# Kernel tuning notes

Hardware: AMD Instinct MI355X
Metric: run time of the kernel (lower is better)

Reference implementation:

```python
import jax, jax.numpy as jnp
from jax import lax
import numpy as np

# ITA requantization params (from init_kwargs)
MQ, SQ = 16384, 8
MK, SK = 16384, 8
MV, SV = 16384, 8
MA, SA = 5, 12
MAV, SAV = 1, 8
MO, SO = 256, 7
NUM_HEADS = 6


def requantize(x, mult, shift, add=0):
    # x * mult, floor-div by 2**shift, add, clamp to int8 range (values kept in float32)
    return jnp.clip(jnp.floor(x * mult / (2.0 ** shift)) + add, -128.0, 127.0)


def ita_softmax(x):
    # x: [B, h, S, Skv] float32 with integer values in [-128, 127]
    B, h, S, Skv = x.shape
    width, bits = 16, 8
    eps_max = 32.0 * bits / (2 ** bits)  # range_scale * bits / 2**bits = 1.0
    groups = Skv // width
    x3 = x.reshape(B * h, S, Skv).astype(jnp.int32)
    # [groups, BH, S, width] for streaming scan over key chunks
    chunks = x3.reshape(B * h, S, groups, width).transpose(2, 0, 1, 3)

    def step(carry, chunk):
        exp_partial_sum, global_max = carry
        current_max = chunk.max(axis=-1)
        update = current_max > global_max
        max_shift = jnp.floor((current_max - global_max).astype(jnp.float32) * eps_max + 0.5).astype(jnp.int32)
        shift_sum = jnp.where(update, max_shift, 0)
        global_max = jnp.where(update, current_max, global_max)
        diff = global_max[..., None] - chunk  # >= 0
        shift = jnp.floor(diff.astype(jnp.float32) * eps_max + 0.5).astype(jnp.int32)
        # 2**bits >> shift  (256 >> shift; any shift >= 9 yields 0, clamp to keep shift defined)
        exp_sum = jnp.sum(jnp.right_shift(jnp.int32(256), jnp.minimum(shift, 31)), axis=-1).astype(jnp.int32)
        exp_partial_sum = jnp.right_shift(exp_partial_sum, jnp.minimum(shift_sum, 31)) + exp_sum
        return (exp_partial_sum, global_max), None

    init = (jnp.zeros((B * h, S), jnp.int32), jnp.full((B * h, S), -128, jnp.int32))
    (exp_partial_sum, global_max), _ = lax.scan(step, init, chunks)

    # (2**bits - 1) * 2**bits = 65280
    inv = jnp.floor(65280.0 / exp_partial_sum.astype(jnp.float32)).astype(jnp.int32)
    diff = global_max[..., None] - x3  # >= 0
    shift = jnp.floor(diff.astype(jnp.float32) * eps_max + 0.5).astype(jnp.int32)
    res = jnp.right_shift(inv[..., None], jnp.minimum(shift, 31)).astype(jnp.uint8)
    return res.reshape(B, h, S, Skv)


def setup_inputs() -> dict:
    key = jax.random.key(0)
    ks = jax.random.split(key, 9)
    B, N, D = 4, 2048, 384
    scale = 1.0 / np.sqrt(D)
    return {
        "x": jax.random.normal(ks[0], (B, N, D), jnp.float32),
        "wq": jax.random.normal(ks[1], (D, D), jnp.float32) * scale,
        "bq": jnp.zeros((D,), jnp.float32),
        "wk": jax.random.normal(ks[2], (D, D), jnp.float32) * scale,
        "bk": jnp.zeros((D,), jnp.float32),
        "wv": jax.random.normal(ks[3], (D, D), jnp.float32) * scale,
        "bv": jnp.zeros((D,), jnp.float32),
        "wo": jax.random.normal(ks[4], (D, D), jnp.float32) * scale,
        "bo": jnp.zeros((D,), jnp.float32),
        "H": 64,
        "W": 32,
    }


def reference(x, wq, bq, wk, bk, wv, bv, wo, bo, H, W):
    B, N, _ = x.shape
    h = NUM_HEADS
    hd = wq.shape[0] // h

    Q = requantize(x @ wq.T + bq, MQ, SQ)
    K = requantize(x @ wk.T + bk, MK, SK)
    V = requantize(x @ wv.T + bv, MV, SV)

    Qr = Q.reshape(B, N, h, hd).transpose(0, 2, 1, 3)  # [B,h,N,hd]
    Kr = K.reshape(B, N, h, hd).transpose(0, 2, 1, 3)
    Vr = V.reshape(B, N, h, hd).transpose(0, 2, 1, 3)

    logits = requantize(jnp.einsum('bhqd,bhkd->bhqk', Qr, Kr), MA, SA)
    attn = ita_softmax(logits)  # uint8 [B,h,N,N]
    ctx = requantize(jnp.einsum('bhqk,bhkd->bhqd', attn.astype(jnp.float32), Vr), MAV, SAV)
    ctx = ctx.transpose(0, 2, 1, 3).reshape(B, N, h * hd)
    out = requantize(ctx @ wo.T + bo, MO, SO)
    return out
```

## Files before the change

### kernel.cpp

```cpp
#include <hip/hip_runtime.h>
#include <stdint.h>

#define NB 4
#define NN 2048
#define ND 384
#define NH 6
#define HD 64
#define ROWS (NB * NN)

typedef int v4i __attribute__((ext_vector_type(4)));
typedef float v4f __attribute__((ext_vector_type(4)));
typedef float v2f __attribute__((ext_vector_type(2)));
typedef _Float16 half_t;
typedef half_t v8h __attribute__((ext_vector_type(8)));

#define PK_FMA_LO(accv, ap, bp)                                            \
    asm("v_pk_fma_f32 %0, %1, %2, %0 op_sel:[0,0,0] op_sel_hi:[0,1,1]"     \
        : "+v"(accv) : "v"(ap), "v"(bp))
#define PK_FMA_HI(accv, ap, bp)                                            \
    asm("v_pk_fma_f32 %0, %1, %2, %0 op_sel:[1,0,0] op_sel_hi:[1,1,1]"     \
        : "+v"(accv) : "v"(ap), "v"(bp))

__global__ __launch_bounds__(256) void qkv_gemm_kernel(
    const float* __restrict__ X,
    const float* __restrict__ Wq, const float* __restrict__ Wk, const float* __restrict__ Wv,
    const float* __restrict__ Bq, const float* __restrict__ Bk, const float* __restrict__ Bv,
    int8_t* __restrict__ Q8, int8_t* __restrict__ K8, int8_t* __restrict__ V8T,
    int* __restrict__ CS)
{
    __shared__ __attribute__((aligned(16))) float As[2][16][132];
    __shared__ __attribute__((aligned(16))) float Bs[2][16][100];
    __shared__ int lcol[96];

    const int t = threadIdx.x;
    const int tx = t & 15;
    const int ty = t >> 4;
    const int row0 = blockIdx.x * 128;
    const int m = blockIdx.y >> 2;
    const int cl0 = (blockIdx.y & 3) * 96;
    const float* W = (m == 0) ? Wq : (m == 1) ? Wk : Wv;
    const float* Bi = (m == 0) ? Bq : (m == 1) ? Bk : Bv;

    const int sr = t >> 1;
    const int sk = (t & 1) * 8;
    const float* xp = X + (size_t)(row0 + sr) * ND + sk;
    const float* wp = W + (size_t)(cl0 + sr) * ND + sk;

    v2f acc[8][3];
#pragma unroll
    for (int i = 0; i < 8; ++i)
#pragma unroll
        for (int p = 0; p < 3; ++p) acc[i][p] = (v2f)0.0f;

    float4 xa0 = *(const float4*)xp;
    float4 xa1 = *(const float4*)(xp + 4);
    float4 wb0, wb1;
    if (t < 192) { wb0 = *(const float4*)wp; wb1 = *(const float4*)(wp + 4); }

    int cur = 0;
    for (int k0 = 0; k0 < ND; k0 += 16) {
        As[cur][sk + 0][sr] = xa0.x; As[cur][sk + 1][sr] = xa0.y;
        As[cur][sk + 2][sr] = xa0.z; As[cur][sk + 3][sr] = xa0.w;
        As[cur][sk + 4][sr] = xa1.x; As[cur][sk + 5][sr] = xa1.y;
        As[cur][sk + 6][sr] = xa1.z; As[cur][sk + 7][sr] = xa1.w;
        if (t < 192) {
            Bs[cur][sk + 0][sr] = wb0.x; Bs[cur][sk + 1][sr] = wb0.y;
            Bs[cur][sk + 2][sr] = wb0.z; Bs[cur][sk + 3][sr] = wb0.w;
            Bs[cur][sk + 4][sr] = wb1.x; Bs[cur][sk + 5][sr] = wb1.y;
            Bs[cur][sk + 6][sr] = wb1.z; Bs[cur][sk + 7][sr] = wb1.w;
        }

        if (k0 + 16 < ND) {
            xa0 = *(const float4*)(xp + k0 + 16);
            xa1 = *(const float4*)(xp + k0 + 20);
            if (t < 192) {
                wb0 = *(const float4*)(wp + k0 + 16);
                wb1 = *(const float4*)(wp + k0 + 20);
            }
        }
        __syncthreads();

#pragma unroll
        for (int kk = 0; kk < 16; ++kk) {
            const v2f* arp  = (const v2f*)&As[cur][kk][ty * 8];
            const v2f* brp  = (const v2f*)&Bs[cur][kk][tx * 4];
            const v2f* brp2 = (const v2f*)&Bs[cur][kk][64 + tx * 2];
            v2f ap0 = arp[0], ap1 = arp[1], ap2 = arp[2], ap3 = arp[3];
            v2f bp0 = brp[0], bp1 = brp[1], bp2 = brp2[0];

            PK_FMA_LO(acc[0][0], ap0, bp0); PK_FMA_LO(acc[0][1], ap0, bp1);
            PK_FMA_LO(acc[0][2], ap0, bp2);
            PK_FMA_HI(acc[1][0], ap0, bp0); PK_FMA_HI(acc[1][1], ap0, bp1);
            PK_FMA_HI(acc[1][2], ap0, bp2);

            PK_FMA_LO(acc[2][0], ap1, bp0); PK_FMA_LO(acc[2][1], ap1, bp1);
            PK_FMA_LO(acc[2][2], ap1, bp2);
            PK_FMA_HI(acc[3][0], ap1, bp0); PK_FMA_HI(acc[3][1], ap1, bp1);
            PK_FMA_HI(acc[3][2], ap1, bp2);

            PK_FMA_LO(acc[4][0], ap2, bp0); PK_FMA_LO(acc[4][1], ap2, bp1);
            PK_FMA_LO(acc[4][2], ap2, bp2);
            PK_FMA_HI(acc[5][0], ap2, bp0); PK_FMA_HI(acc[5][1], ap2, bp1);
            PK_FMA_HI(acc[5][2], ap2, bp2);

            PK_FMA_LO(acc[6][0], ap3, bp0); PK_FMA_LO(acc[6][1], ap3, bp1);
            PK_FMA_LO(acc[6][2], ap3, bp2);
            PK_FMA_HI(acc[7][0], ap3, bp0); PK_FMA_HI(acc[7][1], ap3, bp1);
            PK_FMA_HI(acc[7][2], ap3, bp2);
        }
        cur ^= 1;
    }

    const int bidx = row0 >> 11;
    const int n0 = row0 & 2047;
    const int c1 = cl0 + tx * 4;
    const int c2 = cl0 + 64 + tx * 2;
    const int h1 = c1 >> 6, d1 = c1 & 63;
    const int h2 = c2 >> 6, d2 = c2 & 63;

    if (m != 2) {
        int8_t* Out = (m == 0) ? Q8 : K8;
        const float b1a = Bi[c1], b1b = Bi[c1 + 1], b1c = Bi[c1 + 2], b1d = Bi[c1 + 3];
        const float b2a = Bi[c2], b2b = Bi[c2 + 1];
#pragma unroll
        for (int i = 0; i < 8; ++i) {
            const int n = n0 + ty * 8 + i;
            float v0 = acc[i][0][0] + b1a, v1 = acc[i][0][1] + b1b;
            float v2 = acc[i][1][0] + b1c, v3 = acc[i][1][1] + b1d;
            int q0 = max(-128, min(127, (int)floorf(v0 * 64.0f)));
            int q1 = max(-128, min(127, (int)floorf(v1 * 64.0f)));
            int q2 = max(-128, min(127, (int)floorf(v2 * 64.0f)));
            int q3 = max(-128, min(127, (int)floorf(v3 * 64.0f)));
            uint32_t w = (uint32_t)(q0 & 255) | ((uint32_t)(q1 & 255) << 8)
                       | ((uint32_t)(q2 & 255) << 16) | ((uint32_t)(q3 & 255) << 24);
            *(uint32_t*)(Out + (((size_t)(bidx * NH + h1) * NN) + n) * HD + d1) = w;

            float v4 = acc[i][2][0] + b2a, v5 = acc[i][2][1] + b2b;
            int q4 = max(-128, min(127, (int)floorf(v4 * 64.0f)));
            int q5 = max(-128, min(127, (int)floorf(v5 * 64.0f)));
            *(uint16_t*)(Out + (((size_t)(bidx * NH + h2) * NN) + n) * HD + d2) =
                (uint16_t)((q4 & 255) | ((q5 & 255) << 8));
        }
    } else {
        if (t < 96) lcol[t] = 0;
        __syncthreads();
#pragma unroll
        for (int j = 0; j < 6; ++j) {
            const int lc = (j < 4) ? (tx * 4 + j) : (64 + tx * 2 + (j - 4));
            const int col = cl0 + lc;
            const int head = col >> 6, d = col & 63;
            const float bias = Bi[col];
            int s = 0;
            uint32_t w[2] = {0u, 0u};
#pragma unroll
            for (int i = 0; i < 8; ++i) {
                float v = ((j < 4) ? acc[i][j >> 1][j & 1] : acc[i][2][j - 4]) + bias;
                int qv = (int)floorf(v * 64.0f);
                qv = max(-128, min(127, qv));
                s += qv;
                w[i >> 2] |= (uint32_t)(qv & 255) << (8 * (i & 3));
            }
            uint32_t* dst = (uint32_t*)(V8T + ((size_t)(bidx * NH + head) * HD + d) * NN
                                        + n0 + ty * 8);
            dst[0] = w[0];
            dst[1] = w[1];
            atomicAdd(&lcol[lc], s);
        }
        __syncthreads();
        if (t < 96) {
            const int col = cl0 + t;
            atomicAdd(&CS[(bidx * NH + (col >> 6)) * 64 + (col & 63)], lcol[t]);
        }
    }
}

__global__ __launch_bounds__(256, 4) void attn_kernel(
    const int8_t* __restrict__ Q8, const int8_t* __restrict__ K8,
    const int8_t* __restrict__ V8T, const int* __restrict__ colsum,
    int8_t* __restrict__ CTX8)
{
    __shared__ int Lp[128 * 68];
    __shared__ int gmaxw[128 * 4];
    __shared__ int esumw[128 * 8];

    const int t = threadIdx.x;
    const int wid = t >> 6;
    const int lane = t & 63;
    const int quad = lane >> 4;
    const int l15 = lane & 15;
    const int bh = blockIdx.y;
    const int q0 = blockIdx.x * 16;
    const size_t base = (size_t)bh * NN * HD;
    const v4i zero = {0, 0, 0, 0};

    v4i afrag = *(const v4i*)(Q8 + base + (size_t)(q0 + l15) * HD + quad * 16);
    {
        const int8_t* kp = K8 + base + (size_t)(wid * 32 * 16 + l15) * HD + quad * 16;
        v4i bfrag = *(const v4i*)kp;
        for (int kt = wid * 32; kt < wid * 32 + 32; ++kt) {
            v4i cur = bfrag;
            kp += 16 * HD;
            bfrag = *(const v4i*)kp;
            v4i d = __builtin_amdgcn_mfma_i32_16x16x64_i8(afrag, cur, zero, 0, 0, 0);
            int e[4];
#pragma unroll
            for (int r = 0; r < 4; ++r) {
                int lg = (d[r] * 5) >> 12;
                e[r] = min(127, max(-128, lg));
            }
            int p01 = __builtin_amdgcn_perm(e[1], e[0], 0x00000400);
            int p23 = __builtin_amdgcn_perm(e[3], e[2], 0x00000400);
            Lp[kt * 68 + quad * 16 + l15] = __builtin_amdgcn_perm(p23, p01, 0x05040100);
        }
    }
    __syncthreads();

    int wb[2][16];
#pragma unroll
    for (int it = 0; it < 2; ++it) {
        const int task = t + it * 256;
        const int g = task & 127, qq = task >> 7;
        const int* p = &Lp[g * 68 + qq * 16];
#pragma unroll
        for (int a = 0; a < 4; ++a) {
            v4i v = *(const v4i*)&p[a * 4];
            wb[it][a * 4 + 0] = v.x; wb[it][a * 4 + 1] = v.y;
            wb[it][a * 4 + 2] = v.z; wb[it][a * 4 + 3] = v.w;
        }
        int mx[4];
#pragma unroll
        for (int b = 0; b < 4; ++b) {
            int m = INT_MIN;
#pragma unroll
            for (int j = 0; j < 16; ++j)
                m = max(m, (int)((unsigned)wb[it][j] << (8 * (3 - b))));
            mx[b] = m;
        }
        int p01 = __builtin_amdgcn_perm(mx[1], mx[0], 0x00000703);
        int p23 = __builtin_amdgcn_perm(mx[3], mx[2], 0x00000703);
        gmaxw[g * 4 + qq] = __builtin_amdgcn_perm(p23, p01, 0x05040100);
    }
    __syncthreads();

    if (t < 16) {
        const int wq = t >> 2, bq = 8 * (t & 3);
        int8_t* gb = (int8_t*)gmaxw;
        int m = -128;
        for (int g = 0; g < 128; ++g) {
            int x = (int)(int8_t)(gmaxw[g * 4 + wq] >> bq);
            m = max(m, x);
            gb[g * 16 + t] = (int8_t)m;
        }
    }
    __syncthreads();

#pragma unroll
    for (int it = 0; it < 2; ++it) {
        const int task = t + it * 256;
        const int g = task & 127, qq = task >> 7;
        const int pw = gmaxw[g * 4 + qq];
        uint32_t sp[2] = {0u, 0u};
#pragma unroll
        for (int b = 0; b < 4; ++b) {
            const int M = (int)(int8_t)(pw >> (8 * b));
            const int cb = 8 - M;
            int s = 0;
#pragma unroll
            for (int j = 0; j < 16; ++j) {
                int x = (int)(int8_t)(wb[it][j] >> (8 * b));
                int tt = x + cb;
                s += (tt >= 0) ? (1 << tt) : 0;
            }
            sp[b >> 1] |= (uint32_t)s << (16 * (b & 1));
        }
        *(int2*)&esumw[g * 8 + qq * 2] = make_int2((int)sp[0], (int)sp[1]);
    }
    __syncthreads();

    if (t < 16) {
        const int8_t* gb = (const int8_t*)gmaxw;
        const uint16_t* eb = (const uint16_t*)esumw;
        int E = 0, Mp = -128;
        for (int g = 0; g < 128; ++g) {
            int m = (int)gb[g * 16 + t];
            int d = m - Mp; if (d > 31) d = 31;
            E = (E >> d) + (int)eb[g * 16 + t];
            Mp = m;
        }
        Lp[t * 68 + 64] = 65280 / E;
        Lp[t * 68 + 65] = Mp;
    }
    __syncthreads();

    const int inv_l = Lp[l15 * 68 + 64];
    const int c24 = 24 - Lp[l15 * 68 + 65];
    const int sh8 = 8 * (l15 & 3);
    v4i accs[4] = {zero, zero, zero, zero};
    const int8_t* vtb = V8T + base;

    v4i bf[4];
    {
        const int koff0 = wid * 8 * 64 + quad * 16;
#pragma unroll
        for (int dtb = 0; dtb < 4; ++dtb)
            bf[dtb] = *(const v4i*)(vtb + (size_t)(dtb * 16 + l15) * NN + koff0);
    }
    for (int kc = wid * 8; kc < wid * 8 + 8; ++kc) {
        const int* lp = &Lp[(kc * 4 + quad) * 68 + (l15 >> 2) * 16];
        v4i w4[4];
#pragma unroll
        for (int r = 0; r < 4; ++r) w4[r] = *(const v4i*)&lp[4 * r];

        v4i b0 = bf[0], b1 = bf[1], b2 = bf[2], b3 = bf[3];
        const int koffn = (kc + 1) * 64 + quad * 16;
#pragma unroll
        for (int dtb = 0; dtb < 4; ++dtb)
            bf[dtb] = *(const v4i*)(vtb + (size_t)(dtb * 16 + l15) * NN + koffn);

        v4i a;
#pragma unroll
        for (int r = 0; r < 4; ++r) {
            int u[4];
#pragma unroll
            for (int c = 0; c < 4; ++c) {
                int x = (int)(int8_t)(w4[r][c] >> sh8);
                int t1 = x + c24;
                t1 = (t1 < 0) ? 0 : t1;
                u[c] = (int)((unsigned)inv_l << t1);
            }
            int p01 = __builtin_amdgcn_perm(u[1], u[0], 0x00000703);
            int p23 = __builtin_amdgcn_perm(u[3], u[2], 0x00000703);
            a[r] = __builtin_amdgcn_perm(p23, p01, 0x05040100) ^ (int)0x80808080u;
        }
        accs[0] = __builtin_amdgcn_mfma_i32_16x16x64_i8(a, b0, accs[0], 0, 0, 0);
        accs[1] = __builtin_amdgcn_mfma_i32_16x16x64_i8(a, b1, accs[1], 0, 0, 0);
        accs[2] = __builtin_amdgcn_mfma_i32_16x16x64_i8(a, b2, accs[2], 0, 0, 0);
        accs[3] = __builtin_amdgcn_mfma_i32_16x16x64_i8(a, b3, accs[3], 0, 0, 0);
    }
    __syncthreads();

    if (wid > 0) {
#pragma unroll
        for (int dt = 0; dt < 4; ++dt)
#pragma unroll
            for (int r = 0; r < 4; ++r)
                Lp[(dt * 4 + r) * 192 + (wid - 1) * 64 + lane] = accs[dt][r];
    }
    __syncthreads();
    if (wid == 0) {
        const int bb = bh / NH, hh = bh % NH;
        const int* cs = &colsum[bh * 64];
#pragma unroll
        for (int dt = 0; dt < 4; ++dt) {
            const int dcol = dt * 16 + l15;
            const int corr = cs[dcol] << 7;
#pragma unroll
            for (int r = 0; r < 4; ++r) {
                const int i = dt * 4 + r;
                int val = accs[dt][r]
                        + Lp[i * 192 + 0 * 64 + lane]
                        + Lp[i * 192 + 1 * 64 + lane]
                        + Lp[i * 192 + 2 * 64 + lane];
                const int q = q0 + quad * 4 + r;
                val = (val + corr) >> 8;
                val = min(127, max(-128, val));
                CTX8[((size_t)(bb * NN + q)) * ND + hh * HD + dcol] = (int8_t)val;
            }
        }
    }
}

__global__ __launch_bounds__(256) void out_gemm_kernel(
    const int8_t* __restrict__ CTX8, const float* __restrict__ Wo,
    const float* __restrict__ Bo, float* __restrict__ out)
{
    __shared__ __attribute__((aligned(16))) half_t AH[64 * 40];
    __shared__ __attribute__((aligned(16))) half_t BH[64 * 40];
    __shared__ __attribute__((aligned(16))) half_t BL[64 * 40];

    const int t = threadIdx.x;
    const int wid = t >> 6;
    const int lane = t & 63;
    const int quad = lane >> 4;
    const int l15 = lane & 15;
    const int row0 = blockIdx.x * 64;
    const int c0 = blockIdx.y * 64;

    const int arow = t >> 2;
    const int akb = (t & 3) * 8;
    const int8_t* ap = CTX8 + (size_t)(row0 + arow) * ND + akb;
    const float* wp = Wo + (size_t)(c0 + arow) * ND + akb;

    v4f accH[4], accL[4];
#pragma unroll
    for (int ct = 0; ct < 4; ct++) { accH[ct] = (v4f)0.0f; accL[ct] = (v4f)0.0f; }

    for (int k0 = 0; k0 < ND; k0 += 32) {
        int2 a8 = *(const int2*)(ap + k0);
        float4 w0 = *(const float4*)(wp + k0);
        float4 w1 = *(const float4*)(wp + k0 + 4);
        float wsrc[8] = {w0.x, w0.y, w0.z, w0.w, w1.x, w1.y, w1.z, w1.w};

        __syncthreads();
        v8h av, wh8, wl8;
#pragma unroll
        for (int u = 0; u < 4; u++) {
            av[u]     = (half_t)(float)(int)(int8_t)((a8.x >> (8 * u)) & 0xFF);
            av[4 + u] = (half_t)(float)(int)(int8_t)((a8.y >> (8 * u)) & 0xFF);
        }
#pragma unroll
        for (int u = 0; u < 8; u++) {
            float x = wsrc[u];
            half_t h = (half_t)x;
            wh8[u] = h;
            wl8[u] = (half_t)((x - (float)h) * 2048.0f);
        }
        *(v8h*)&AH[arow * 40 + akb] = av;
        *(v8h*)&BH[arow * 40 + akb] = wh8;
        *(v8h*)&BL[arow * 40 + akb] = wl8;
        __syncthreads();

        v8h af = *(const v8h*)&AH[(wid * 16 + l15) * 40 + quad * 8];
#pragma unroll
        for (int ct = 0; ct < 4; ct++) {
            v8h bh8 = *(const v8h*)&BH[(ct * 16 + l15) * 40 + quad * 8];
            v8h bl8 = *(const v8h*)&BL[(ct * 16 + l15) * 40 + quad * 8];
            accH[ct] = __builtin_amdgcn_mfma_f32_16x16x32_f16(af, bh8, accH[ct], 0, 0, 0);
            accL[ct] = __builtin_amdgcn_mfma_f32_16x16x32_f16(af, bl8, accL[ct], 0, 0, 0);
        }
    }

    const float inv2048 = 4.8828125e-4f;
#pragma unroll
    for (int ct = 0; ct < 4; ct++) {
        const int c = c0 + ct * 16 + l15;
        const float bias = Bo[c];
#pragma unroll
        for (int r = 0; r < 4; r++) {
            const int row = row0 + wid * 16 + quad * 4 + r;
            float v = accH[ct][r] + accL[ct][r] * inv2048 + bias;
            float rq = floorf(v * 2.0f);
            rq = fminf(fmaxf(rq, -128.0f), 127.0f);
            out[(size_t)row * ND + c] = rq;
        }
    }
}

extern "C" void kernel_launch(void* const* d_in, const int* in_sizes, int n_in,
                              void* d_out, int out_size, void* d_ws, size_t ws_size,
                              hipStream_t stream)
{
    const float* x  = (const float*)d_in[0];
    const float* wq = (const float*)d_in[1];
    const float* bq = (const float*)d_in[2];
    const float* wk = (const float*)d_in[3];
    const float* bk = (const float*)d_in[4];
    const float* wv = (const float*)d_in[5];
    const float* bv = (const float*)d_in[6];
    const float* wo = (const float*)d_in[7];
    const float* bo = (const float*)d_in[8];
    float* out = (float*)d_out;

    const size_t MAT = (size_t)ROWS * ND;
    int8_t* Q8  = (int8_t*)d_ws;
    int8_t* K8  = Q8 + MAT;
    int8_t* V8T = K8 + MAT;
    int8_t* C8  = V8T + MAT;
    int*    CS  = (int*)(C8 + MAT);

    hipMemsetAsync(CS, 0, (size_t)NB * NH * 64 * sizeof(int), stream);
    qkv_gemm_kernel<<<dim3(ROWS / 128, 12), 256, 0, stream>>>(
        x, wq, wk, wv, bq, bk, bv, Q8, K8, V8T, CS);
    attn_kernel<<<dim3(NN / 16, NB * NH), 256, 0, stream>>>(Q8, K8, V8T, CS, C8);
    out_gemm_kernel<<<dim3(ROWS / 64, ND / 64), 256, 0, stream>>>(C8, wo, bo, out);
}
```

Before: 268.3 us.

## Pre-split Wo into fp16 hi/lo once and load MFMA operands directly from global

Adds a small kernel that converts Wo into fp16 high and scaled low parts once per call, so the output GEMM no longer converts weights in every block. The output GEMM drops its shared-memory staging and both barriers, with each lane loading its A and B MFMA fragments straight from global memory and L2. Separately, the QKV GEMM gets a launch-bounds occupancy hint of 3 blocks per CU. The cost is an extra launch and more redundant global loads of weight fragments per wave, in place of shared-memory reuse.

```diff
diff --git a/kernel.cpp b/kernel.cpp
--- a/kernel.cpp
+++ b/kernel.cpp
@@ -21,7 +21,7 @@
     asm("v_pk_fma_f32 %0, %1, %2, %0 op_sel:[1,0,0] op_sel_hi:[1,1,1]"     \
         : "+v"(accv) : "v"(ap), "v"(bp))
 
-__global__ __launch_bounds__(256) void qkv_gemm_kernel(
+__global__ __launch_bounds__(256, 3) void qkv_gemm_kernel(
     const float* __restrict__ X,
     const float* __restrict__ Wq, const float* __restrict__ Wk, const float* __restrict__ Wv,
     const float* __restrict__ Bq, const float* __restrict__ Bk, const float* __restrict__ Bv,
@@ -370,14 +370,21 @@
     }
 }
 
+__global__ __launch_bounds__(256) void wo_convert_kernel(
+    const float* __restrict__ Wo, half_t* __restrict__ WoH, half_t* __restrict__ WoL)
+{
+    const int idx = blockIdx.x * 256 + threadIdx.x;
+    float x = Wo[idx];
+    half_t h = (half_t)x;
+    WoH[idx] = h;
+    WoL[idx] = (half_t)((x - (float)h) * 2048.0f);
+}
+
 __global__ __launch_bounds__(256) void out_gemm_kernel(
-    const int8_t* __restrict__ CTX8, const float* __restrict__ Wo,
-    const float* __restrict__ Bo, float* __restrict__ out)
+    const int8_t* __restrict__ CTX8, const half_t* __restrict__ WoH,
+    const half_t* __restrict__ WoL, const float* __restrict__ Bo,
+    float* __restrict__ out)
 {
-    __shared__ __attribute__((aligned(16))) half_t AH[64 * 40];
-    __shared__ __attribute__((aligned(16))) half_t BH[64 * 40];
-    __shared__ __attribute__((aligned(16))) half_t BL[64 * 40];
-
     const int t = threadIdx.x;
     const int wid = t >> 6;
     const int lane = t & 63;
@@ -386,10 +393,10 @@
     const int row0 = blockIdx.x * 64;
     const int c0 = blockIdx.y * 64;
 
-    const int arow = t >> 2;
-    const int akb = (t & 3) * 8;
-    const int8_t* ap = CTX8 + (size_t)(row0 + arow) * ND + akb;
-    const float* wp = Wo + (size_t)(c0 + arow) * ND + akb;
+    const int arow = row0 + wid * 16 + l15;
+    const int8_t* ap = CTX8 + (size_t)arow * ND + quad * 8;
+    const half_t* whp = WoH + (size_t)(c0 + l15) * ND + quad * 8;
+    const half_t* wlp = WoL + (size_t)(c0 + l15) * ND + quad * 8;
 
     v4f accH[4], accL[4];
 #pragma unroll
@@ -397,34 +404,16 @@
 
     for (int k0 = 0; k0 < ND; k0 += 32) {
         int2 a8 = *(const int2*)(ap + k0);
-        float4 w0 = *(const float4*)(wp + k0);
-        float4 w1 = *(const float4*)(wp + k0 + 4);
-        float wsrc[8] = {w0.x, w0.y, w0.z, w0.w, w1.x, w1.y, w1.z, w1.w};
-
-        __syncthreads();
-        v8h av, wh8, wl8;
+        v8h af;
 #pragma unroll
         for (int u = 0; u < 4; u++) {
-            av[u]     = (half_t)(float)(int)(int8_t)((a8.x >> (8 * u)) & 0xFF);
-            av[4 + u] = (half_t)(float)(int)(int8_t)((a8.y >> (8 * u)) & 0xFF);
-        }
-#pragma unroll
-        for (int u = 0; u < 8; u++) {
-            float x = wsrc[u];
-            half_t h = (half_t)x;
-            wh8[u] = h;
-            wl8[u] = (half_t)((x - (float)h) * 2048.0f);
-        }
-        *(v8h*)&AH[arow * 40 + akb] = av;
-        *(v8h*)&BH[arow * 40 + akb] = wh8;
-        *(v8h*)&BL[arow * 40 + akb] = wl8;
-        __syncthreads();
-
-        v8h af = *(const v8h*)&AH[(wid * 16 + l15) * 40 + quad * 8];
+            af[u]     = (half_t)(float)(int)(int8_t)((a8.x >> (8 * u)) & 0xFF);
+            af[4 + u] = (half_t)(float)(int)(int8_t)((a8.y >> (8 * u)) & 0xFF);
+        }
 #pragma unroll
         for (int ct = 0; ct < 4; ct++) {
-            v8h bh8 = *(const v8h*)&BH[(ct * 16 + l15) * 40 + quad * 8];
-            v8h bl8 = *(const v8h*)&BL[(ct * 16 + l15) * 40 + quad * 8];
+            v8h bh8 = *(const v8h*)(whp + (size_t)(ct * 16) * ND + k0);
+            v8h bl8 = *(const v8h*)(wlp + (size_t)(ct * 16) * ND + k0);
             accH[ct] = __builtin_amdgcn_mfma_f32_16x16x32_f16(af, bh8, accH[ct], 0, 0, 0);
             accL[ct] = __builtin_amdgcn_mfma_f32_16x16x32_f16(af, bl8, accL[ct], 0, 0, 0);
         }
@@ -467,10 +456,13 @@
     int8_t* V8T = K8 + MAT;
     int8_t* C8  = V8T + MAT;
     int*    CS  = (int*)(C8 + MAT);
+    half_t* WoH = (half_t*)(CS + NB * NH * 64);
+    half_t* WoL = WoH + (size_t)ND * ND;
 
     hipMemsetAsync(CS, 0, (size_t)NB * NH * 64 * sizeof(int), stream);
+    wo_convert_kernel<<<dim3((ND * ND) / 256), 256, 0, stream>>>(wo, WoH, WoL);
     qkv_gemm_kernel<<<dim3(ROWS / 128, 12), 256, 0, stream>>>(
         x, wq, wk, wv, bq, bk, bv, Q8, K8, V8T, CS);
     attn_kernel<<<dim3(NN / 16, NB * NH), 256, 0, stream>>>(Q8, K8, V8T, CS, C8);
-    out_gemm_kernel<<<dim3(ROWS / 64, ND / 64), 256, 0, stream>>>(C8, wo, bo, out);
+    out_gemm_kernel<<<dim3(ROWS / 64, ND / 64), 256, 0, stream>>>(C8, WoH, WoL, bo, out);
 }
```

After: 288.7 us. +7.6%, slower.
